# Performance work log

Measured on AMD Instinct MI355X. Metric: run time of the kernel, lower is better.

Reference implementation:

```python
import jax, jax.numpy as jnp
import numpy as np

N_NODES = 10000
N_EDGES = 100000
F_NODE = 128
F_EDGE = 16
HEADS = 8
OUT_CH = 128  # per-head channels in PyG TransformerConv
HC = HEADS * OUT_CH


def setup_inputs() -> dict:
    key = jax.random.key(0)
    ks = jax.random.split(key, 12)
    sN = 1.0 / np.sqrt(F_NODE)
    sE = 1.0 / np.sqrt(F_EDGE)
    return {
        "x": jax.random.normal(ks[0], (N_NODES, F_NODE), dtype=jnp.float32),
        "edge_attr": jax.random.normal(ks[1], (N_EDGES, F_EDGE), dtype=jnp.float32),
        "edge_index": jax.random.randint(ks[2], (2, N_EDGES), 0, N_NODES, dtype=jnp.int32),
        "Wq": jax.random.normal(ks[3], (F_NODE, HC), dtype=jnp.float32) * sN,
        "bq": jnp.zeros((HC,), dtype=jnp.float32),
        "Wk": jax.random.normal(ks[4], (F_NODE, HC), dtype=jnp.float32) * sN,
        "bk": jnp.zeros((HC,), dtype=jnp.float32),
        "Wv": jax.random.normal(ks[5], (F_NODE, HC), dtype=jnp.float32) * sN,
        "bv": jnp.zeros((HC,), dtype=jnp.float32),
        "We": jax.random.normal(ks[6], (F_EDGE, HC), dtype=jnp.float32) * sE,  # lin_edge has no bias in PyG
        "Wskip": jax.random.normal(ks[7], (F_NODE, OUT_CH), dtype=jnp.float32) * sN,
        "bskip": jnp.zeros((OUT_CH,), dtype=jnp.float32),
        "Wd": jax.random.normal(ks[8], (OUT_CH, 1), dtype=jnp.float32) * (1.0 / np.sqrt(OUT_CH)),
        "bd": jnp.zeros((1,), dtype=jnp.float32),
    }


def reference(x, edge_attr, edge_index, Wq, bq, Wk, bk, Wv, bv, We, Wskip, bskip, Wd, bd):
    N = x.shape[0]
    src, dst = edge_index[0], edge_index[1]  # messages flow src -> dst

    q = (x @ Wq + bq).reshape(N, HEADS, OUT_CH)
    k = (x @ Wk + bk).reshape(N, HEADS, OUT_CH)
    v = (x @ Wv + bv).reshape(N, HEADS, OUT_CH)
    e = (edge_attr @ We).reshape(-1, HEADS, OUT_CH)  # [E, H, C]

    k_j = k[src] + e                        # [E, H, C]
    alpha = jnp.einsum("ehc,ehc->eh", q[dst], k_j) / np.sqrt(OUT_CH)  # [E, H]

    # segment softmax over destination node
    m = jax.ops.segment_max(alpha, dst, num_segments=N)   # [N, H]
    a = jnp.exp(alpha - m[dst])
    s = jax.ops.segment_sum(a, dst, num_segments=N)       # [N, H]
    alpha_n = a / (s[dst] + 1e-16)                        # [E, H]

    msg = (v[src] + e) * alpha_n[:, :, None]              # [E, H, C]
    out = jax.ops.segment_sum(msg, dst, num_segments=N)   # [N, H, C]

    out = out.mean(axis=1)                                # concat=False -> head average, [N, C]
    out = out + x @ Wskip + bskip                         # root/skip connection
    out = jax.nn.relu(out)
    # dropout is identity at inference
    pooled = out.sum(axis=0)                              # [C]
    return pooled @ Wd + bd                               # [1]
```

## Files before the change

### kernel.cpp

```cpp
#include <hip/hip_runtime.h>

#define N_NODES 10000
#define N_EDGES 100000
#define F_NODE 128
#define HEADS 8
#define HC 1024
#define NCOLS2 2432
#define NB2 (NCOLS2 / 128)
#define SLOT_CAP 48

typedef __attribute__((ext_vector_type(8))) short bf16x8;
typedef __attribute__((ext_vector_type(4))) float f32x4;
typedef __attribute__((ext_vector_type(2))) float f32x2;

__device__ __forceinline__ void atomAddF(float* p, float v) {
    unsafeAtomicAdd(p, v);
}
__device__ __forceinline__ unsigned short f2bf(float f) {
    union { float f; unsigned u; } c; c.f = f;
    unsigned u = c.u + 0x7fffu + ((c.u >> 16) & 1u);
    return (unsigned short)(u >> 16);
}
__device__ __forceinline__ float bLo(unsigned x) {
    union { unsigned u; float f; } c; c.u = x << 16; return c.f;
}
__device__ __forceinline__ float bHi(unsigned x) {
    union { unsigned u; float f; } c; c.u = x & 0xffff0000u; return c.f;
}
__device__ __forceinline__ float bf2f(unsigned short u) {
    union { unsigned u; float f; } c; c.u = ((unsigned)u) << 16; return c.f;
}
__device__ __forceinline__ unsigned pk4fp8(unsigned a, unsigned b) {
    int w = __builtin_amdgcn_cvt_pk_fp8_f32(bLo(a), bHi(a), 0, false);
    w = __builtin_amdgcn_cvt_pk_fp8_f32(bLo(b), bHi(b), w, true);
    return (unsigned)w;
}
__device__ __forceinline__ void dq16(uint4 q, float* f) {
    f32x2 p;
    p = __builtin_amdgcn_cvt_pk_f32_fp8(q.x, false); f[0] = p.x;  f[1] = p.y;
    p = __builtin_amdgcn_cvt_pk_f32_fp8(q.x, true);  f[2] = p.x;  f[3] = p.y;
    p = __builtin_amdgcn_cvt_pk_f32_fp8(q.y, false); f[4] = p.x;  f[5] = p.y;
    p = __builtin_amdgcn_cvt_pk_f32_fp8(q.y, true);  f[6] = p.x;  f[7] = p.y;
    p = __builtin_amdgcn_cvt_pk_f32_fp8(q.z, false); f[8] = p.x;  f[9] = p.y;
    p = __builtin_amdgcn_cvt_pk_f32_fp8(q.z, true);  f[10] = p.x; f[11] = p.y;
    p = __builtin_amdgcn_cvt_pk_f32_fp8(q.w, false); f[12] = p.x; f[13] = p.y;
    p = __builtin_amdgcn_cvt_pk_f32_fp8(q.w, true);  f[14] = p.x; f[15] = p.y;
}
__device__ __forceinline__ void edge_accum(
    uint4 xq4, uint4 vq4, float2 eav, float svv, bool valid,
    const float* gf, float qwx, float qwy, float du_r, float scale,
    float& s_reg, float& t0, float& t1, float* va) {
    float xq[16];
    dq16(xq4, xq);
    float d = eav.x * qwx + eav.y * qwy;
    #pragma unroll
    for (int j = 0; j < 16; ++j) d += gf[j] * xq[j];
    d += __shfl_xor(d, 1); d += __shfl_xor(d, 2); d += __shfl_xor(d, 4);
    float a = __expf((d + du_r + svv) * scale);
    a = valid ? a : 0.f;
    s_reg += a;
    t0 += a * eav.x; t1 += a * eav.y;
    float vq[16];
    dq16(vq4, vq);
    #pragma unroll
    for (int j = 0; j < 16; ++j) va[j] += a * vq[j];
}

#define PREP_A 1250
#define PREP_B (PREP_A + NCOLS2 / 2)
#define PREP_C (PREP_B + 10)
#define PREP_D (PREP_C + 64)
__global__ __launch_bounds__(256) void prep_all(
    const float* __restrict__ x, unsigned short* __restrict__ xb,
    unsigned* __restrict__ xf8, const int* __restrict__ ei,
    int* __restrict__ cnt, int2* __restrict__ slots,
    const float* __restrict__ Wq, const float* __restrict__ Wk,
    const float* __restrict__ Wv, const float* __restrict__ Wskip,
    const float* __restrict__ We, const float* __restrict__ bq,
    const float* __restrict__ bk, const float* __restrict__ bv,
    const float* __restrict__ bskip, unsigned short* __restrict__ wt,
    float* __restrict__ bias, unsigned short* __restrict__ w2t) {
    int tid = threadIdx.x;
    if (blockIdx.x < PREP_A) {
        int i = blockIdx.x * 256 + tid;
        float4 f = ((const float4*)x)[i];
        ushort4 o;
        o.x = f2bf(f.x); o.y = f2bf(f.y); o.z = f2bf(f.z); o.w = f2bf(f.w);
        ((ushort4*)xb)[i] = o;
        int w = __builtin_amdgcn_cvt_pk_fp8_f32(f.x, f.y, 0, false);
        w = __builtin_amdgcn_cvt_pk_fp8_f32(f.z, f.w, w, true);
        xf8[i] = (unsigned)w;
        if (i < N_EDGES) {
            int src = ei[i];
            int dst = ei[N_EDGES + i];
            int pos = atomicAdd(&cnt[dst], 1);
            if (pos < SLOT_CAP) slots[(size_t)dst * SLOT_CAP + pos] = make_int2(src, i);
        }
    } else if (blockIdx.x < PREP_B) {
        __shared__ float wesh[2][128];
        int bi = blockIdx.x - PREP_A;
        int cid = tid >> 7, d = tid & 127;
        int n = 2 * bi + cid;
        float val;
        if (n < 1024) {
            int h = n >> 7, f2 = n & 127;
            wesh[cid][d] = Wk[(size_t)f2 * HC + h * 128 + d];
            __syncthreads();
            const float* wq = Wq + (size_t)d * HC + h * 128;
            float s = 0.f;
            #pragma unroll
            for (int c = 0; c < 128; ++c) s += wq[c] * wesh[cid][c];
            val = s;
        } else if (n < 2048) {
            val = Wv[(size_t)d * HC + (n - 1024)];
        } else if (n < 2176) {
            val = Wskip[(size_t)d * 128 + (n - 2048)];
        } else if (n < 2304) {
            int hf = n - 2176, h = hf >> 4, f = hf & 15;
            wesh[cid][d] = We[(size_t)f * HC + h * 128 + d];
            __syncthreads();
            const float* wq = Wq + (size_t)d * HC + h * 128;
            float s = 0.f;
            #pragma unroll
            for (int c = 0; c < 128; ++c) s += wq[c] * wesh[cid][c];
            val = s;
        } else if (n < 2312) {
            int h = n - 2304;
            wesh[cid][d] = bk[h * 128 + d];
            __syncthreads();
            const float* wq = Wq + (size_t)d * HC + h * 128;
            float s = 0.f;
            #pragma unroll
            for (int c = 0; c < 128; ++c) s += wq[c] * wesh[cid][c];
            val = s;
        } else if (n < 2320) {
            int h = n - 2312;
            wesh[cid][d] = bq[h * 128 + d];
            __syncthreads();
            const float* wk = Wk + (size_t)d * HC + h * 128;
            float s = 0.f;
            #pragma unroll
            for (int c = 0; c < 128; ++c) s += wk[c] * wesh[cid][c];
            val = s;
        } else {
            val = 0.f;
        }
        wt[(size_t)n * 128 + d] = f2bf(val);
    } else if (blockIdx.x < PREP_C) {
        int n = (blockIdx.x - PREP_B) * 256 + tid;
        if (n >= NCOLS2) return;
        float val;
        if (n < 1024) val = 0.f;
        else if (n < 2048) val = bv[n - 1024];
        else if (n < 2176) val = bskip[n - 2048];
        else if (n < 2304) {
            int hf = n - 2176, h = hf >> 4, f = hf & 15;
            float s = 0.f;
            for (int c = 0; c < 128; ++c)
                s += bq[h * 128 + c] * We[(size_t)f * HC + h * 128 + c];
            val = s;
        } else if (n < 2312) {
            int h = n - 2304;
            float s = 0.f;
            for (int c = 0; c < 128; ++c) s += bq[h * 128 + c] * bk[h * 128 + c];
            val = s;
        } else val = 0.f;
        bias[n] = val;
    } else {
        int c = (blockIdx.x - PREP_C) * 2 + (tid >> 7);
        int d = tid & 127;
        int h = d >> 4, f = d & 15;
        w2t[(size_t)c * 128 + d] = f2bf(We[(size_t)f * HC + h * 128 + c] * 0.125f);
    }
}

__global__ __launch_bounds__(256) void gemm_mfma(
    const unsigned short* __restrict__ xb, const unsigned short* __restrict__ wt,
    const float* __restrict__ bias, unsigned char* __restrict__ xgf8,
    unsigned char* __restrict__ vf8, unsigned short* __restrict__ sqb,
    float* __restrict__ du, float* __restrict__ sv) {
    __shared__ unsigned short lds[18432];
    unsigned short (*As)[72] = (unsigned short(*)[72])lds;
    unsigned short (*Bs)[72] = (unsigned short(*)[72])(lds + 9216);
    int tid = threadIdx.x;
    int n0 = blockIdx.x * 128, m0 = blockIdx.y * 128;
    int w = tid >> 6, lane = tid & 63;
    int wm = (w >> 1) * 64, wn = (w & 1) * 64;
    int quad = lane >> 4, l16 = lane & 15;
    f32x4 acc[4][4];
    #pragma unroll
    for (int i = 0; i < 4; ++i)
        #pragma unroll
        for (int j = 0; j < 4; ++j) acc[i][j] = (f32x4){0.f, 0.f, 0.f, 0.f};

    for (int ko = 0; ko < 128; ko += 64) {
        #pragma unroll
        for (int tI = 0; tI < 4; ++tI) {
            int cId = tid + tI * 256;
            int r = cId >> 3, c8 = (cId & 7) << 3;
            int gr = m0 + r;
            uint4 av = make_uint4(0u, 0u, 0u, 0u);
            if (gr < N_NODES)
                av = *(const uint4*)(xb + (size_t)gr * 128 + ko + c8);
            *(uint4*)(&As[r][c8]) = av;
            *(uint4*)(&Bs[r][c8]) =
                *(const uint4*)(wt + (size_t)(n0 + r) * 128 + ko + c8);
        }
        __syncthreads();
        #pragma unroll
        for (int ks = 0; ks < 64; ks += 32) {
            bf16x8 a[4], b[4];
            #pragma unroll
            for (int mt = 0; mt < 4; ++mt)
                a[mt] = *(const bf16x8*)&As[wm + mt * 16 + l16][ks + quad * 8];
            #pragma unroll
            for (int nt = 0; nt < 4; ++nt)
                b[nt] = *(const bf16x8*)&Bs[wn + nt * 16 + l16][ks + quad * 8];
            #pragma unroll
            for (int mt = 0; mt < 4; ++mt)
                #pragma unroll
                for (int nt = 0; nt < 4; ++nt)
                    acc[mt][nt] = __builtin_amdgcn_mfma_f32_16x16x32_bf16(
                        a[mt], b[nt], acc[mt][nt], 0, 0, 0);
        }
        __syncthreads();
    }
    int nt0 = n0 >> 7;
    if (nt0 >= 16) {
        #pragma unroll
        for (int mt = 0; mt < 4; ++mt)
            #pragma unroll
            for (int r = 0; r < 4; ++r) {
                int row = m0 + wm + mt * 16 + quad * 4 + r;
                if (row >= N_NODES) continue;
                #pragma unroll
                for (int nt = 0; nt < 4; ++nt) {
                    int col = n0 + wn + nt * 16 + l16;
                    float val = acc[mt][nt][r] + bias[col];
                    if (col < 2304) {
                        sqb[(size_t)row * 256 + (col - 2048)] = f2bf(val);
                    } else if (col < 2312) {
                        du[(size_t)row * 8 + (col - 2304)] = val;
                    } else if (col < 2320) {
                        sv[(size_t)row * 8 + (col - 2312)] = val;
                    }
                }
            }
    } else {
        unsigned short* wst = lds + w * 4608;
        #pragma unroll
        for (int mt = 0; mt < 4; ++mt)
            #pragma unroll
            for (int r = 0; r < 4; ++r) {
                int rl = mt * 16 + quad * 4 + r;
                #pragma unroll
                for (int nt = 0; nt < 4; ++nt) {
                    int cl = nt * 16 + l16;
                    wst[rl * 72 + cl] = f2bf(acc[mt][nt][r] + bias[n0 + wn + cl]);
                }
            }
        unsigned char* dst = (nt0 < 8) ? xgf8 : vf8;
        int colbase = (n0 & 1023) + wn;
        #pragma unroll
        for (int p = 0; p < 4; ++p) {
            int rl = p * 16 + (lane >> 2);
            int row = m0 + wm + rl;
            if (row < N_NODES) {
                const uint4* sp = (const uint4*)(wst + rl * 72 + (lane & 3) * 16);
                uint4 u0 = sp[0], u1 = sp[1];
                uint4 o;
                o.x = pk4fp8(u0.x, u0.y);
                o.y = pk4fp8(u0.z, u0.w);
                o.z = pk4fp8(u1.x, u1.y);
                o.w = pk4fp8(u1.z, u1.w);
                *(uint4*)(dst + (size_t)row * 1024 + colbase + (lane & 3) * 16) = o;
            }
        }
    }
}

__global__ __launch_bounds__(256) void node_kernel(
    const unsigned char* __restrict__ xgf8, const unsigned char* __restrict__ xf8,
    const unsigned char* __restrict__ vf8, const unsigned short* __restrict__ sqb,
    const float* __restrict__ ea, const float* __restrict__ du,
    const float* __restrict__ sv, const int2* __restrict__ slots,
    const int* __restrict__ cnt, unsigned short* __restrict__ ttb,
    float* __restrict__ hsum) {
    int t = threadIdx.x;
    int w = t >> 6, lane = t & 63;
    int lh = lane & 7, h = lane >> 3;
    const float scale = 0.08838834764831845f;
    int n = blockIdx.x * 4 + w;

    uint4 gq = *(const uint4*)(xgf8 + (size_t)n * 1024 + 16 * lane);
    float gf[16];
    dq16(gq, gf);
    ushort2 qwu = *(const ushort2*)(sqb + (size_t)n * 256 + 128 + h * 16 + 2 * lh);
    float qwx = bf2f(qwu.x), qwy = bf2f(qwu.y);
    float du_r = du[(size_t)n * 8 + h];

    int cn = cnt[n];
    cn = (cn > SLOT_CAP) ? SLOT_CAP : cn;
    int end = cn;
    const int2* sp = slots + (size_t)n * SLOT_CAP;
    float va[16];
    #pragma unroll
    for (int i = 0; i < 16; ++i) va[i] = 0.f;
    float s_reg = 0.f, t0 = 0.f, t1 = 0.f;

    int2 saC = make_int2(0, 0), sbC = make_int2(0, 0);
    uint4 xAC, xBC, vAC, vBC;
    float2 eAC, eBC;
    float svAC = 0.f, svBC = 0.f;
    bool bBC = false;

    if (0 < end) {
        bool bv = (1 < end);
        int i1 = bv ? 1 : 0;
        saC = sp[0]; sbC = sp[i1]; bBC = bv;
        xAC = *(const uint4*)(xf8 + (size_t)saC.x * 128 + lh * 16);
        xBC = *(const uint4*)(xf8 + (size_t)sbC.x * 128 + lh * 16);
        vAC = *(const uint4*)(vf8 + (size_t)saC.x * 1024 + 16 * lane);
        vBC = *(const uint4*)(vf8 + (size_t)sbC.x * 1024 + 16 * lane);
        eAC = *(const float2*)(ea + (size_t)saC.y * 16 + 2 * lh);
        eBC = *(const float2*)(ea + (size_t)sbC.y * 16 + 2 * lh);
        svAC = sv[(size_t)saC.x * 8 + h];
        svBC = sv[(size_t)sbC.x * 8 + h];
    }
    for (int ii = 0; ii < end; ii += 2) {
        int in = ii + 2;
        bool hn = in < end;
        int2 saN = make_int2(0, 0), sbN = make_int2(0, 0);
        uint4 xAN, xBN, vAN, vBN;
        float2 eAN, eBN;
        float svAN = 0.f, svBN = 0.f;
        bool bBN = false;
        if (hn) {
            bool bv = (in + 1 < end);
            int i1 = bv ? in + 1 : in;
            saN = sp[in]; sbN = sp[i1]; bBN = bv;
            xAN = *(const uint4*)(xf8 + (size_t)saN.x * 128 + lh * 16);
            xBN = *(const uint4*)(xf8 + (size_t)sbN.x * 128 + lh * 16);
            vAN = *(const uint4*)(vf8 + (size_t)saN.x * 1024 + 16 * lane);
            vBN = *(const uint4*)(vf8 + (size_t)sbN.x * 1024 + 16 * lane);
            eAN = *(const float2*)(ea + (size_t)saN.y * 16 + 2 * lh);
            eBN = *(const float2*)(ea + (size_t)sbN.y * 16 + 2 * lh);
            svAN = sv[(size_t)saN.x * 8 + h];
            svBN = sv[(size_t)sbN.x * 8 + h];
        }
        edge_accum(xAC, vAC, eAC, svAC, true, gf, qwx, qwy, du_r, scale,
                   s_reg, t0, t1, va);
        edge_accum(xBC, vBC, eBC, svBC, bBC, gf, qwx, qwy, du_r, scale,
                   s_reg, t0, t1, va);
        if (hn) {
            saC = saN; sbC = sbN; bBC = bBN;
            xAC = xAN; xBC = xBN; vAC = vAN; vBC = vBN;
            eAC = eAN; eBC = eBN; svAC = svAN; svBC = svBN;
        }
    }

    float inv = 1.f / (s_reg + 1e-16f);
    ushort2 tw;
    tw.x = f2bf(t0 * inv);
    tw.y = f2bf(t1 * inv);
    *(ushort2*)(ttb + (size_t)n * 128 + h * 16 + 2 * lh) = tw;
    float sc = inv * 0.125f;
    #pragma unroll
    for (int i = 0; i < 16; ++i) {
        float o = va[i] * sc;
        o += __shfl_xor(o, 8);
        o += __shfl_xor(o, 16);
        o += __shfl_xor(o, 32);
        va[i] = o;
    }
    if (lane < 8) {
        float* hp = hsum + (size_t)n * 128 + lane * 16;
        #pragma unroll
        for (int p2 = 0; p2 < 4; ++p2) {
            float4 h4 = make_float4(va[4 * p2], va[4 * p2 + 1],
                                    va[4 * p2 + 2], va[4 * p2 + 3]);
            ((float4*)hp)[p2] = h4;
        }
    }
}

__global__ __launch_bounds__(256) void out_gemm(
    const unsigned short* __restrict__ ttb, const unsigned short* __restrict__ w2t,
    const float* __restrict__ hsum, const unsigned short* __restrict__ sqb,
    float* __restrict__ pooled, int* __restrict__ done,
    const float* __restrict__ Wd, const float* __restrict__ bd,
    float* __restrict__ out) {
    __shared__ unsigned short As[64][136];
    __shared__ float pool_sh[128];
    __shared__ int last_sh;
    int tid = threadIdx.x;
    int m0 = blockIdx.x * 64;
    int w = tid >> 6, lane = tid & 63;
    int wm = (w >> 1) * 32, wn = (w & 1) * 64;
    int quad = lane >> 4, l16 = lane & 15;
    if (tid < 128) pool_sh[tid] = 0.f;
    #pragma unroll
    for (int tI = 0; tI < 4; ++tI) {
        int cId = tid + tI * 256;
        int r = cId >> 4, c8 = (cId & 15) << 3;
        int gr = m0 + r;
        uint4 av = make_uint4(0u, 0u, 0u, 0u);
        if (gr < N_NODES)
            av = *(const uint4*)(ttb + (size_t)gr * 128 + c8);
        *(uint4*)(&As[r][c8]) = av;
    }
    __syncthreads();
    f32x4 acc[2][4];
    #pragma unroll
    for (int i = 0; i < 2; ++i)
        #pragma unroll
        for (int j = 0; j < 4; ++j) acc[i][j] = (f32x4){0.f, 0.f, 0.f, 0.f};

    const unsigned short* bb = w2t + (size_t)(wn + l16) * 128 + quad * 8;
    #pragma unroll
    for (int ks = 0; ks < 128; ks += 32) {
        bf16x8 a[2], b[4];
        #pragma unroll
        for (int mt = 0; mt < 2; ++mt)
            a[mt] = *(const bf16x8*)&As[wm + mt * 16 + l16][ks + quad * 8];
        #pragma unroll
        for (int nt = 0; nt < 4; ++nt)
            b[nt] = *(const bf16x8*)(bb + (size_t)nt * 16 * 128 + ks);
        #pragma unroll
        for (int mt = 0; mt < 2; ++mt)
            #pragma unroll
            for (int nt = 0; nt < 4; ++nt)
                acc[mt][nt] = __builtin_amdgcn_mfma_f32_16x16x32_bf16(
                    a[mt], b[nt], acc[mt][nt], 0, 0, 0);
    }
    float pl[4] = {0.f, 0.f, 0.f, 0.f};
    #pragma unroll
    for (int mt = 0; mt < 2; ++mt) {
        #pragma unroll
        for (int r = 0; r < 4; ++r) {
            int row = m0 + wm + mt * 16 + quad * 4 + r;
            if (row >= N_NODES) continue;
            #pragma unroll
            for (int nt = 0; nt < 4; ++nt) {
                int col = wn + nt * 16 + l16;
                float val = acc[mt][nt][r] + hsum[(size_t)row * 128 + col]
                            + bf2f(sqb[(size_t)row * 256 + col]);
                pl[nt] += fmaxf(val, 0.f);
            }
        }
    }
    #pragma unroll
    for (int nt = 0; nt < 4; ++nt)
        atomicAdd(&pool_sh[wn + nt * 16 + l16], pl[nt]);
    __syncthreads();
    if (tid < 128) atomAddF(&pooled[tid], pool_sh[tid]);
    __threadfence();
    if (tid == 0) last_sh = (atomicAdd(done, 1) == (int)gridDim.x - 1);
    __syncthreads();
    if (last_sh && tid < 64) {
        float p0 = __hip_atomic_load(&pooled[2 * tid], __ATOMIC_RELAXED,
                                     __HIP_MEMORY_SCOPE_AGENT);
        float p1 = __hip_atomic_load(&pooled[2 * tid + 1], __ATOMIC_RELAXED,
                                     __HIP_MEMORY_SCOPE_AGENT);
        float vv = p0 * Wd[2 * tid] + p1 * Wd[2 * tid + 1];
        vv += __shfl_xor(vv, 1);  vv += __shfl_xor(vv, 2);  vv += __shfl_xor(vv, 4);
        vv += __shfl_xor(vv, 8);  vv += __shfl_xor(vv, 16); vv += __shfl_xor(vv, 32);
        if (tid == 0) out[0] = vv + bd[0];
    }
}

extern "C" void kernel_launch(void* const* d_in, const int* in_sizes, int n_in,
                              void* d_out, int out_size, void* d_ws, size_t ws_size,
                              hipStream_t stream) {
    const float* x     = (const float*)d_in[0];
    const float* eattr = (const float*)d_in[1];
    const int*   ei    = (const int*)d_in[2];
    const float* Wq    = (const float*)d_in[3];
    const float* bq    = (const float*)d_in[4];
    const float* Wk    = (const float*)d_in[5];
    const float* bk    = (const float*)d_in[6];
    const float* Wv    = (const float*)d_in[7];
    const float* bv    = (const float*)d_in[8];
    const float* We    = (const float*)d_in[9];
    const float* Wskip = (const float*)d_in[10];
    const float* bskip = (const float*)d_in[11];
    const float* Wd    = (const float*)d_in[12];
    const float* bd    = (const float*)d_in[13];
    float* out = (float*)d_out;

    char* ws = (char*)d_ws;
    unsigned char*  xgf8 = (unsigned char*)(ws + 0);
    unsigned char*  vf8  = (unsigned char*)(ws + 10240000);
    unsigned short* sqb  = (unsigned short*)(ws + 20480000);
    float* hsum = (float*)(ws + 25600000);
    unsigned short* xb   = (unsigned short*)(ws + 30720000);
    unsigned short* ttb  = xb;
    unsigned*       xf8  = (unsigned*)(ws + 33280000);
    float* du   = (float*)(ws + 34560000);
    float* sv   = (float*)(ws + 34880000);
    unsigned short* wt   = (unsigned short*)(ws + 35200000);
    float* bias = (float*)(ws + 35822592);
    unsigned short* w2t  = (unsigned short*)(ws + 35832320);
    int* cnt    = (int*)(ws + 35865088);
    float* pooled = (float*)(ws + 35905088);
    int* done   = (int*)(ws + 35905600);
    int2* slots = (int2*)(ws + 35905616);

    hipMemsetAsync(cnt, 0, 40000 + 512 + 16, stream);

    prep_all<<<PREP_D, 256, 0, stream>>>(
        x, xb, xf8, ei, cnt, slots, Wq, Wk, Wv, Wskip, We, bq, bk, bv, bskip,
        wt, bias, w2t);

    gemm_mfma<<<dim3(NB2, (N_NODES + 127) / 128), 256, 0, stream>>>(
        xb, wt, bias, xgf8, vf8, sqb, du, sv);

    node_kernel<<<N_NODES / 4, 256, 0, stream>>>(
        xgf8, (const unsigned char*)xf8, vf8, sqb, eattr, du, sv, slots, cnt,
        ttb, hsum);

    out_gemm<<<(N_NODES + 63) / 64, 256, 0, stream>>>(
        ttb, w2t, hsum, sqb, pooled, done, Wd, bd, out);
}
```

Measured before the change: 191.6 us.

## Deepen node-kernel gather prefetch, pack FP32 math, and tile weight-fold prep

The node kernel now keeps two pairs of edge gathers in flight using a double-buffered prefetch instead of one. It also uses packed two-wide float math (v_pk_fma style) for the fp8 dot products and value accumulation, and makes the node index and edge count wave-uniform via readfirstlane so address math runs on scalar registers with 32-bit offsets. In prep, the Wq·Wk and Wq·We weight folds now stage Wq panels in shared memory with coalesced loads instead of strided per-thread global reads. The cost is higher register pressure from the larger in-flight buffers and a larger static shared allocation in the prep kernel.

```diff
diff --git a/kernel.cpp b/kernel.cpp
--- a/kernel.cpp
+++ b/kernel.cpp
@@ -35,35 +35,47 @@
     w = __builtin_amdgcn_cvt_pk_fp8_f32(bLo(b), bHi(b), w, true);
     return (unsigned)w;
 }
-__device__ __forceinline__ void dq16(uint4 q, float* f) {
+__device__ __forceinline__ void dq16v(uint4 q, f32x2* f) {
+    f[0] = __builtin_amdgcn_cvt_pk_f32_fp8(q.x, false);
+    f[1] = __builtin_amdgcn_cvt_pk_f32_fp8(q.x, true);
+    f[2] = __builtin_amdgcn_cvt_pk_f32_fp8(q.y, false);
+    f[3] = __builtin_amdgcn_cvt_pk_f32_fp8(q.y, true);
+    f[4] = __builtin_amdgcn_cvt_pk_f32_fp8(q.z, false);
+    f[5] = __builtin_amdgcn_cvt_pk_f32_fp8(q.z, true);
+    f[6] = __builtin_amdgcn_cvt_pk_f32_fp8(q.w, false);
+    f[7] = __builtin_amdgcn_cvt_pk_f32_fp8(q.w, true);
+}
+__device__ __forceinline__ void edge_accum2(
+    uint4 xq4, uint4 vq4, float2 eav, float svv, bool valid,
+    const f32x2* gf2, float qwx, float qwy, float du_r, float scale,
+    float& s_reg, float& t0, float& t1, f32x2* va2) {
+    f32x2 dac;
+    dac.x = eav.x * qwx;
+    dac.y = eav.y * qwy;
     f32x2 p;
-    p = __builtin_amdgcn_cvt_pk_f32_fp8(q.x, false); f[0] = p.x;  f[1] = p.y;
-    p = __builtin_amdgcn_cvt_pk_f32_fp8(q.x, true);  f[2] = p.x;  f[3] = p.y;
-    p = __builtin_amdgcn_cvt_pk_f32_fp8(q.y, false); f[4] = p.x;  f[5] = p.y;
-    p = __builtin_amdgcn_cvt_pk_f32_fp8(q.y, true);  f[6] = p.x;  f[7] = p.y;
-    p = __builtin_amdgcn_cvt_pk_f32_fp8(q.z, false); f[8] = p.x;  f[9] = p.y;
-    p = __builtin_amdgcn_cvt_pk_f32_fp8(q.z, true);  f[10] = p.x; f[11] = p.y;
-    p = __builtin_amdgcn_cvt_pk_f32_fp8(q.w, false); f[12] = p.x; f[13] = p.y;
-    p = __builtin_amdgcn_cvt_pk_f32_fp8(q.w, true);  f[14] = p.x; f[15] = p.y;
-}
-__device__ __forceinline__ void edge_accum(
-    uint4 xq4, uint4 vq4, float2 eav, float svv, bool valid,
-    const float* gf, float qwx, float qwy, float du_r, float scale,
-    float& s_reg, float& t0, float& t1, float* va) {
-    float xq[16];
-    dq16(xq4, xq);
-    float d = eav.x * qwx + eav.y * qwy;
-    #pragma unroll
-    for (int j = 0; j < 16; ++j) d += gf[j] * xq[j];
+    p = __builtin_amdgcn_cvt_pk_f32_fp8(xq4.x, false); dac += gf2[0] * p;
+    p = __builtin_amdgcn_cvt_pk_f32_fp8(xq4.x, true);  dac += gf2[1] * p;
+    p = __builtin_amdgcn_cvt_pk_f32_fp8(xq4.y, false); dac += gf2[2] * p;
+    p = __builtin_amdgcn_cvt_pk_f32_fp8(xq4.y, true);  dac += gf2[3] * p;
+    p = __builtin_amdgcn_cvt_pk_f32_fp8(xq4.z, false); dac += gf2[4] * p;
+    p = __builtin_amdgcn_cvt_pk_f32_fp8(xq4.z, true);  dac += gf2[5] * p;
+    p = __builtin_amdgcn_cvt_pk_f32_fp8(xq4.w, false); dac += gf2[6] * p;
+    p = __builtin_amdgcn_cvt_pk_f32_fp8(xq4.w, true);  dac += gf2[7] * p;
+    float d = dac.x + dac.y;
     d += __shfl_xor(d, 1); d += __shfl_xor(d, 2); d += __shfl_xor(d, 4);
     float a = __expf((d + du_r + svv) * scale);
     a = valid ? a : 0.f;
     s_reg += a;
     t0 += a * eav.x; t1 += a * eav.y;
-    float vq[16];
-    dq16(vq4, vq);
-    #pragma unroll
-    for (int j = 0; j < 16; ++j) va[j] += a * vq[j];
+    f32x2 av; av.x = a; av.y = a;
+    p = __builtin_amdgcn_cvt_pk_f32_fp8(vq4.x, false); va2[0] += av * p;
+    p = __builtin_amdgcn_cvt_pk_f32_fp8(vq4.x, true);  va2[1] += av * p;
+    p = __builtin_amdgcn_cvt_pk_f32_fp8(vq4.y, false); va2[2] += av * p;
+    p = __builtin_amdgcn_cvt_pk_f32_fp8(vq4.y, true);  va2[3] += av * p;
+    p = __builtin_amdgcn_cvt_pk_f32_fp8(vq4.z, false); va2[4] += av * p;
+    p = __builtin_amdgcn_cvt_pk_f32_fp8(vq4.z, true);  va2[5] += av * p;
+    p = __builtin_amdgcn_cvt_pk_f32_fp8(vq4.w, false); va2[6] += av * p;
+    p = __builtin_amdgcn_cvt_pk_f32_fp8(vq4.w, true);  va2[7] += av * p;
 }
 
 #define PREP_A 1250
@@ -80,6 +92,8 @@
     const float* __restrict__ bk, const float* __restrict__ bv,
     const float* __restrict__ bskip, unsigned short* __restrict__ wt,
     float* __restrict__ bias, unsigned short* __restrict__ w2t) {
+    __shared__ float wesh[2][128];
+    __shared__ float wqsh[64][129];
     int tid = threadIdx.x;
     if (blockIdx.x < PREP_A) {
         int i = blockIdx.x * 256 + tid;
@@ -97,55 +111,64 @@
             if (pos < SLOT_CAP) slots[(size_t)dst * SLOT_CAP + pos] = make_int2(src, i);
         }
     } else if (blockIdx.x < PREP_B) {
-        __shared__ float wesh[2][128];
         int bi = blockIdx.x - PREP_A;
         int cid = tid >> 7, d = tid & 127;
         int n = 2 * bi + cid;
-        float val;
-        if (n < 1024) {
-            int h = n >> 7, f2 = n & 127;
-            wesh[cid][d] = Wk[(size_t)f2 * HC + h * 128 + d];
-            __syncthreads();
-            const float* wq = Wq + (size_t)d * HC + h * 128;
+        bool panel = (n < 1024) || (n >= 2176 && n < 2304);
+        if (panel) {
+            int h = (n < 1024) ? (n >> 7) : ((n - 2176) >> 4);
+            if (n < 1024) {
+                int f2 = n & 127;
+                wesh[cid][d] = Wk[(size_t)f2 * HC + h * 128 + d];
+            } else {
+                int f = (n - 2176) & 15;
+                wesh[cid][d] = We[(size_t)f * HC + h * 128 + d];
+            }
             float s = 0.f;
-            #pragma unroll
-            for (int c = 0; c < 128; ++c) s += wq[c] * wesh[cid][c];
-            val = s;
-        } else if (n < 2048) {
-            val = Wv[(size_t)d * HC + (n - 1024)];
-        } else if (n < 2176) {
-            val = Wskip[(size_t)d * 128 + (n - 2048)];
-        } else if (n < 2304) {
-            int hf = n - 2176, h = hf >> 4, f = hf & 15;
-            wesh[cid][d] = We[(size_t)f * HC + h * 128 + d];
-            __syncthreads();
-            const float* wq = Wq + (size_t)d * HC + h * 128;
-            float s = 0.f;
-            #pragma unroll
-            for (int c = 0; c < 128; ++c) s += wq[c] * wesh[cid][c];
-            val = s;
-        } else if (n < 2312) {
-            int h = n - 2304;
-            wesh[cid][d] = bk[h * 128 + d];
-            __syncthreads();
-            const float* wq = Wq + (size_t)d * HC + h * 128;
-            float s = 0.f;
-            #pragma unroll
-            for (int c = 0; c < 128; ++c) s += wq[c] * wesh[cid][c];
-            val = s;
-        } else if (n < 2320) {
-            int h = n - 2312;
-            wesh[cid][d] = bq[h * 128 + d];
-            __syncthreads();
-            const float* wk = Wk + (size_t)d * HC + h * 128;
-            float s = 0.f;
-            #pragma unroll
-            for (int c = 0; c < 128; ++c) s += wk[c] * wesh[cid][c];
-            val = s;
+            int c_t = tid & 63, r_t = tid >> 6;
+            #pragma unroll 2
+            for (int half = 0; half < 2; ++half) {
+                #pragma unroll
+                for (int rr = 0; rr < 32; ++rr) {
+                    int r = rr * 4 + r_t;
+                    wqsh[c_t][r] = Wq[(size_t)r * HC + h * 128 + half * 64 + c_t];
+                }
+                __syncthreads();
+                #pragma unroll 16
+                for (int cc = 0; cc < 64; ++cc)
+                    s += wqsh[cc][d] * wesh[cid][half * 64 + cc];
+                __syncthreads();
+            }
+            wt[(size_t)n * 128 + d] = f2bf(s);
         } else {
-            val = 0.f;
-        }
-        wt[(size_t)n * 128 + d] = f2bf(val);
+            float val;
+            if (n < 2048) {
+                val = Wv[(size_t)d * HC + (n - 1024)];
+            } else if (n < 2176) {
+                val = Wskip[(size_t)d * 128 + (n - 2048)];
+            } else if (n < 2312) {
+                int h = n - 2304;
+                wesh[cid][d] = bk[h * 128 + d];
+                __syncthreads();
+                const float* wq = Wq + (size_t)d * HC + h * 128;
+                float s = 0.f;
+                #pragma unroll
+                for (int c = 0; c < 128; ++c) s += wq[c] * wesh[cid][c];
+                val = s;
+            } else if (n < 2320) {
+                int h = n - 2312;
+                wesh[cid][d] = bq[h * 128 + d];
+                __syncthreads();
+                const float* wk = Wk + (size_t)d * HC + h * 128;
+                float s = 0.f;
+                #pragma unroll
+                for (int c = 0; c < 128; ++c) s += wk[c] * wesh[cid][c];
+                val = s;
+            } else {
+                val = 0.f;
+            }
+            wt[(size_t)n * 128 + d] = f2bf(val);
+        }
     } else if (blockIdx.x < PREP_C) {
         int n = (blockIdx.x - PREP_B) * 256 + tid;
         if (n >= NCOLS2) return;
@@ -290,73 +313,77 @@
     int w = t >> 6, lane = t & 63;
     int lh = lane & 7, h = lane >> 3;
     const float scale = 0.08838834764831845f;
-    int n = blockIdx.x * 4 + w;
+    int n = __builtin_amdgcn_readfirstlane(blockIdx.x * 4 + w);
 
     uint4 gq = *(const uint4*)(xgf8 + (size_t)n * 1024 + 16 * lane);
-    float gf[16];
-    dq16(gq, gf);
+    f32x2 gf2[8];
+    dq16v(gq, gf2);
     ushort2 qwu = *(const ushort2*)(sqb + (size_t)n * 256 + 128 + h * 16 + 2 * lh);
     float qwx = bf2f(qwu.x), qwy = bf2f(qwu.y);
     float du_r = du[(size_t)n * 8 + h];
 
     int cn = cnt[n];
     cn = (cn > SLOT_CAP) ? SLOT_CAP : cn;
-    int end = cn;
+    cn = __builtin_amdgcn_readfirstlane(cn);
     const int2* sp = slots + (size_t)n * SLOT_CAP;
-    float va[16];
-    #pragma unroll
-    for (int i = 0; i < 16; ++i) va[i] = 0.f;
+    const unsigned char* eab = (const unsigned char*)ea;
+
+    unsigned xoff = lh * 16u;
+    unsigned voff = lane * 16u;
+    unsigned eoff = lh * 8u;
+
+    f32x2 va2[8];
+    #pragma unroll
+    for (int i = 0; i < 8; ++i) va2[i] = (f32x2){0.f, 0.f};
     float s_reg = 0.f, t0 = 0.f, t1 = 0.f;
 
-    int2 saC = make_int2(0, 0), sbC = make_int2(0, 0);
-    uint4 xAC, xBC, vAC, vBC;
-    float2 eAC, eBC;
-    float svAC = 0.f, svBC = 0.f;
-    bool bBC = false;
-
-    if (0 < end) {
-        bool bv = (1 < end);
-        int i1 = bv ? 1 : 0;
-        saC = sp[0]; sbC = sp[i1]; bBC = bv;
-        xAC = *(const uint4*)(xf8 + (size_t)saC.x * 128 + lh * 16);
-        xBC = *(const uint4*)(xf8 + (size_t)sbC.x * 128 + lh * 16);
-        vAC = *(const uint4*)(vf8 + (size_t)saC.x * 1024 + 16 * lane);
-        vBC = *(const uint4*)(vf8 + (size_t)sbC.x * 1024 + 16 * lane);
-        eAC = *(const float2*)(ea + (size_t)saC.y * 16 + 2 * lh);
-        eBC = *(const float2*)(ea + (size_t)sbC.y * 16 + 2 * lh);
-        svAC = sv[(size_t)saC.x * 8 + h];
-        svBC = sv[(size_t)sbC.x * 8 + h];
-    }
-    for (int ii = 0; ii < end; ii += 2) {
-        int in = ii + 2;
-        bool hn = in < end;
-        int2 saN = make_int2(0, 0), sbN = make_int2(0, 0);
-        uint4 xAN, xBN, vAN, vBN;
-        float2 eAN, eBN;
-        float svAN = 0.f, svBN = 0.f;
-        bool bBN = false;
-        if (hn) {
-            bool bv = (in + 1 < end);
-            int i1 = bv ? in + 1 : in;
-            saN = sp[in]; sbN = sp[i1]; bBN = bv;
-            xAN = *(const uint4*)(xf8 + (size_t)saN.x * 128 + lh * 16);
-            xBN = *(const uint4*)(xf8 + (size_t)sbN.x * 128 + lh * 16);
-            vAN = *(const uint4*)(vf8 + (size_t)saN.x * 1024 + 16 * lane);
-            vBN = *(const uint4*)(vf8 + (size_t)sbN.x * 1024 + 16 * lane);
-            eAN = *(const float2*)(ea + (size_t)saN.y * 16 + 2 * lh);
-            eBN = *(const float2*)(ea + (size_t)sbN.y * 16 + 2 * lh);
-            svAN = sv[(size_t)saN.x * 8 + h];
-            svBN = sv[(size_t)sbN.x * 8 + h];
-        }
-        edge_accum(xAC, vAC, eAC, svAC, true, gf, qwx, qwy, du_r, scale,
-                   s_reg, t0, t1, va);
-        edge_accum(xBC, vBC, eBC, svBC, bBC, gf, qwx, qwy, du_r, scale,
-                   s_reg, t0, t1, va);
-        if (hn) {
-            saC = saN; sbC = sbN; bBC = bBN;
-            xAC = xAN; xBC = xBN; vAC = vAN; vBC = vBN;
-            eAC = eAN; eBC = eBN; svAC = svAN; svBC = svBN;
-        }
+    if (cn > 0) {
+        int np = (cn + 1) >> 1;
+        uint4 x0A = {}, x0B = {}, v0A = {}, v0B = {};
+        uint4 x1A = {}, x1B = {}, v1A = {}, v1B = {};
+        float2 e0A = {}, e0B = {}, e1A = {}, e1B = {};
+        float sv0A = 0.f, sv0B = 0.f, sv1A = 0.f, sv1B = 0.f;
+        bool m0B = false, m1B = false;
+
+#define LOADP(xA, xB, vA, vB, eA, eB, svA, svB, mB, pp) do {                    \
+        int _p = (pp);                                                          \
+        if (_p < np) {                                                          \
+            int _i0 = 2 * _p;                                                   \
+            bool _mb = (_i0 + 1) < cn;                                          \
+            int2 _sa = sp[_i0];                                                 \
+            int2 _sb = sp[_mb ? _i0 + 1 : _i0];                                 \
+            mB = _mb;                                                           \
+            xA = *(const uint4*)(xf8 + (((unsigned)_sa.x) << 7) + xoff);        \
+            xB = *(const uint4*)(xf8 + (((unsigned)_sb.x) << 7) + xoff);        \
+            vA = *(const uint4*)(vf8 + (((unsigned)_sa.x) << 10) + voff);       \
+            vB = *(const uint4*)(vf8 + (((unsigned)_sb.x) << 10) + voff);       \
+            eA = *(const float2*)(eab + (((unsigned)_sa.y) << 6) + eoff);       \
+            eB = *(const float2*)(eab + (((unsigned)_sb.y) << 6) + eoff);       \
+            svA = sv[(((unsigned)_sa.x) << 3) + h];                             \
+            svB = sv[(((unsigned)_sb.x) << 3) + h];                             \
+        }                                                                       \
+    } while (0)
+
+        LOADP(x0A, x0B, v0A, v0B, e0A, e0B, sv0A, sv0B, m0B, 0);
+        LOADP(x1A, x1B, v1A, v1B, e1A, e1B, sv1A, sv1B, m1B, 1);
+        int p = 0;
+        while (true) {
+            if (p >= np) break;
+            edge_accum2(x0A, v0A, e0A, sv0A, true, gf2, qwx, qwy, du_r, scale,
+                        s_reg, t0, t1, va2);
+            edge_accum2(x0B, v0B, e0B, sv0B, m0B, gf2, qwx, qwy, du_r, scale,
+                        s_reg, t0, t1, va2);
+            LOADP(x0A, x0B, v0A, v0B, e0A, e0B, sv0A, sv0B, m0B, p + 2);
+            ++p;
+            if (p >= np) break;
+            edge_accum2(x1A, v1A, e1A, sv1A, true, gf2, qwx, qwy, du_r, scale,
+                        s_reg, t0, t1, va2);
+            edge_accum2(x1B, v1B, e1B, sv1B, m1B, gf2, qwx, qwy, du_r, scale,
+                        s_reg, t0, t1, va2);
+            LOADP(x1A, x1B, v1A, v1B, e1A, e1B, sv1A, sv1B, m1B, p + 2);
+            ++p;
+        }
+#undef LOADP
     }
 
     float inv = 1.f / (s_reg + 1e-16f);
@@ -365,6 +392,9 @@
     tw.y = f2bf(t1 * inv);
     *(ushort2*)(ttb + (size_t)n * 128 + h * 16 + 2 * lh) = tw;
     float sc = inv * 0.125f;
+    float va[16];
+    #pragma unroll
+    for (int i = 0; i < 8; ++i) { va[2 * i] = va2[i].x; va[2 * i + 1] = va2[i].y; }
     #pragma unroll
     for (int i = 0; i < 16; ++i) {
         float o = va[i] * sc;
```

Measured after the change: 178.3 us. 6.9% less time.
